# Optimization experiments

Measured on AMD Instinct MI355X. Metric: run time of the kernel, lower is better.

## Reference

```python
import jax, jax.numpy as jnp
import numpy as np

N_NODES = 100000
N_EDGES = 1600000
IN_DIM, HID_DIM, OUT_DIM = 128, 256, 128


def gcn_conv(x, src, dst, W, b, n):
    # PyG GCNConv: linear transform, add self-loops, symmetric normalization,
    # scatter-sum aggregation over destination nodes, then bias.
    h = x @ W  # [n, d_out]
    loops = jnp.arange(n, dtype=src.dtype)
    s = jnp.concatenate([src, loops])
    d = jnp.concatenate([dst, loops])
    deg = jax.ops.segment_sum(jnp.ones_like(d, dtype=h.dtype), d, num_segments=n)
    dinv = jnp.where(deg > 0, jax.lax.rsqrt(deg), 0.0)
    norm = dinv[s] * dinv[d]  # [E+n]
    msg = h[s] * norm[:, None]  # gather + scale
    out = jax.ops.segment_sum(msg, d, num_segments=n)  # scatter-reduce
    return out + b


def layer_norm(x, gamma, beta, eps=1e-5):
    mu = jnp.mean(x, axis=-1, keepdims=True)
    var = jnp.mean(jnp.square(x - mu), axis=-1, keepdims=True)
    return (x - mu) * jax.lax.rsqrt(var + eps) * gamma + beta


def setup_inputs() -> dict:
    key = jax.random.key(0)
    ks = jax.random.split(key, 8)
    x = jax.random.normal(ks[0], (N_NODES, IN_DIM), dtype=jnp.float32)
    edge_index = jax.random.randint(ks[1], (2, N_EDGES), 0, N_NODES, dtype=jnp.int64)
    W1 = jax.random.normal(ks[2], (IN_DIM, HID_DIM), dtype=jnp.float32) * (1.0 / np.sqrt(IN_DIM))
    b1 = jnp.zeros((HID_DIM,), dtype=jnp.float32)
    W2 = jax.random.normal(ks[3], (HID_DIM, OUT_DIM), dtype=jnp.float32) * (1.0 / np.sqrt(HID_DIM))
    b2 = jnp.zeros((OUT_DIM,), dtype=jnp.float32)
    gamma = jnp.ones((OUT_DIM,), dtype=jnp.float32)
    beta = jnp.zeros((OUT_DIM,), dtype=jnp.float32)
    return {"x": x, "edge_index": edge_index, "W1": W1, "b1": b1,
            "W2": W2, "b2": b2, "gamma": gamma, "beta": beta}


def reference(x, edge_index, W1, b1, W2, b2, gamma, beta):
    n = x.shape[0]
    src, dst = edge_index[0], edge_index[1]
    h = gcn_conv(x, src, dst, W1, b1, n)
    h = jax.nn.relu(h)
    # dropout(p=0.1) is identity in eval mode
    h = gcn_conv(h, src, dst, W2, b2, n)
    return layer_norm(h, gamma, beta)
```

## Files before the change

kernel.cpp:

```cpp
#include <hip/hip_runtime.h>
#include <hip/hip_fp16.h>
#include <stdint.h>

#define N_NODES 100000
#define N_EDGES 1600000
#define IN_DIM  128
#define HID_DIM 256
#define OUT_DIM 128
#define RS 264
#define NBUCK 391
#define EPB   4096
#define PADB  5120
#define PB    391
#define WB    256

typedef __attribute__((ext_vector_type(8))) _Float16 f16x8;
typedef __attribute__((ext_vector_type(4))) float f32x4;

__device__ __forceinline__ int clampi(int v) {
    v = v < 0 ? 0 : v;
    return v >= N_NODES ? N_NODES - 1 : v;
}
__device__ __forceinline__ float2 h2f2(uint32_t u) {
    union { uint32_t u; __half2 h; } c; c.u = u;
    return __half22float2(c.h);
}
__device__ __forceinline__ uint32_t packh(float a, float b) {
    union { __half2 h; uint32_t u; } c; c.h = __floats2half2_rn(a, b);
    return c.u;
}
__device__ __forceinline__ uint16_t f2h(float a) {
    union { __half h; uint16_t s; } c; c.h = __float2half_rn(a);
    return c.s;
}

__device__ __forceinline__ int src_at(const int* ei, int isI64, int e) {
    return clampi(isI64 ? ei[2 * (size_t)e] : ei[e]);
}
__device__ __forceinline__ int dst_at(const int* ei, int isI64, int e) {
    return clampi(isI64 ? ei[2 * (size_t)N_EDGES + 2 * (size_t)e]
                        : ei[(size_t)N_EDGES + e]);
}


__global__ __launch_bounds__(256) void partition_kernel(const int* __restrict__ ei,
                                                        int* __restrict__ cursor,
                                                        uint32_t* __restrict__ recs,
                                                        const float* __restrict__ W1,
                                                        uint16_t* __restrict__ W1t,
                                                        const float* __restrict__ W2,
                                                        uint16_t* __restrict__ W2t) {
    if (blockIdx.x >= PB) {
        int idx = (blockIdx.x - PB) * 256 + threadIdx.x;
        if (idx < IN_DIM * HID_DIM) {
            int k = idx / HID_DIM, n = idx - k * HID_DIM;
            W1t[n * IN_DIM + k] = f2h(W1[idx]);
        } else {
            int j = idx - IN_DIM * HID_DIM;
            int k = j / OUT_DIM, n = j - k * OUT_DIM;
            W2t[n * HID_DIM + k] = f2h(W2[j]);
        }
        return;
    }
    __shared__ int hist[NBUCK];
    __shared__ int gBase[NBUCK];
    __shared__ int s_flag;
    int tid = threadIdx.x;
    if (tid == 0) {
        int z = 1;
        #pragma unroll
        for (int i = 0; i < 16; ++i)
            if (ei[2 * i + 1] != 0) z = 0;
        s_flag = z;
    }
    for (int b = tid; b < NBUCK; b += 256) hist[b] = 0;
    __syncthreads();
    int isI64 = s_flag;
    int base = blockIdx.x * EPB;
    int srcs[16], dsts[16], slots[16];
    #pragma unroll
    for (int r = 0; r < 16; ++r) {
        int e = base + r * 256 + tid;
        slots[r] = -1;
        srcs[r] = 0; dsts[r] = 0;
        if (e < N_EDGES) {
            srcs[r] = src_at(ei, isI64, e);
            dsts[r] = dst_at(ei, isI64, e);
            slots[r] = atomicAdd(&hist[dsts[r] >> 8], 1);
        }
    }
    __syncthreads();
    for (int b = tid; b < NBUCK; b += 256)
        if (hist[b] > 0) gBase[b] = atomicAdd(&cursor[b], hist[b]);
    __syncthreads();
    #pragma unroll
    for (int r = 0; r < 16; ++r) {
        if (slots[r] >= 0) {
            int b = dsts[r] >> 8;
            int pos = gBase[b] + slots[r];
            if (pos < PADB)
                recs[(size_t)b * PADB + pos] =
                    ((uint32_t)srcs[r] << 8) | (uint32_t)(dsts[r] & 255);
        }
    }
}


__global__ __launch_bounds__(256) void build_kernel(const uint32_t* __restrict__ recs,
                                                    const int* __restrict__ cursor,
                                                    int* __restrict__ row_ptr,
                                                    float* __restrict__ dinv,
                                                    int* __restrict__ colv) {
    __shared__ int cnt[256];
    __shared__ int lofs[256];
    __shared__ int cur[256];
    __shared__ int wsum[8];
    int b = blockIdx.x, tid = threadIdx.x;
    int lane = tid & 63, wv = tid >> 6;
    int nb = cursor[b]; if (nb > PADB) nb = PADB;
    int pv = 0;
    for (int j = tid; j < b; j += 256) {
        int c = cursor[j];
        pv += (c > PADB) ? PADB : c;
    }
    #pragma unroll
    for (int o = 32; o > 0; o >>= 1) pv += __shfl_xor(pv, o, 64);
    cnt[tid] = 0; cur[tid] = 0;
    if (lane == 0) wsum[wv] = pv;
    __syncthreads();
    int cbase = wsum[0] + wsum[1] + wsum[2] + wsum[3];
    uint32_t rr[20];
    #pragma unroll
    for (int r = 0; r < 20; ++r) {
        int i = r * 256 + tid;
        rr[r] = 0xFFFFFFFFu;
        if (i < nb) {
            rr[r] = recs[(size_t)b * PADB + i];
            atomicAdd(&cnt[rr[r] & 255], 1);
        }
    }
    __syncthreads();
    int v = cnt[tid];
    int inc = v;
    #pragma unroll
    for (int o = 1; o < 64; o <<= 1) {
        int t = __shfl_up(inc, o, 64);
        if (lane >= o) inc += t;
    }
    if (lane == 63) wsum[4 + wv] = inc;
    __syncthreads();
    int woff = 0;
    #pragma unroll
    for (int w = 0; w < 4; ++w) if (w < wv) woff += wsum[4 + w];
    int excl = woff + inc - v;
    lofs[tid] = excl;
    int node = b * 256 + tid;
    if (node < N_NODES) {
        row_ptr[node] = cbase + excl;
        dinv[node] = rsqrtf((float)(v + 1));
    }
    if (b == NBUCK - 1 && tid == 0) row_ptr[N_NODES] = cbase + nb;
    __syncthreads();
    #pragma unroll
    for (int r = 0; r < 20; ++r) {
        if (rr[r] != 0xFFFFFFFFu) {
            int id = (int)(rr[r] & 255);
            int slot = atomicAdd(&cur[id], 1);
            colv[cbase + lofs[id] + slot] = (int)(rr[r] >> 8);
        }
    }
}


__global__ __launch_bounds__(256) void xscale_kernel(const float* __restrict__ x,
                                                     const float* __restrict__ dinv,
                                                     uint2* __restrict__ xs16) {
    int idx = blockIdx.x * 256 + threadIdx.x;
    if (idx < N_NODES * 32) {
        float d = dinv[idx >> 5];
        float4 v = ((const float4*)x)[idx];
        uint2 o;
        o.x = packh(d * v.x, d * v.y);
        o.y = packh(d * v.z, d * v.w);
        xs16[idx] = o;
    }
}


template<bool LN>
__global__ __launch_bounds__(256) void agg_kernel(const uint4* __restrict__ rows,
                                                  const int* __restrict__ row_ptr,
                                                  const int* __restrict__ colv,
                                                  const float* __restrict__ dinv,
                                                  const float* __restrict__ bias,
                                                  const float* __restrict__ gamma,
                                                  const float* __restrict__ beta,
                                                  float* __restrict__ out,
                                                  uint4* __restrict__ out16) {
    int node = blockIdx.x * 16 + (threadIdx.x >> 4);
    if (node >= N_NODES) return;
    int l = threadIdx.x & 15;
    const char* base = (const char*)rows + ((unsigned)l << 4);
    float di = dinv[node];
    float acc[8];
    {
        uint4 u = *(const uint4*)(base + ((unsigned)node << 8));
        float2 f0 = h2f2(u.x), f1 = h2f2(u.y), f2 = h2f2(u.z), f3 = h2f2(u.w);
        acc[0] = f0.x; acc[1] = f0.y; acc[2] = f1.x; acc[3] = f1.y;
        acc[4] = f2.x; acc[5] = f2.y; acc[6] = f3.x; acc[7] = f3.y;
    }
    int e = row_ptr[node], e1 = row_ptr[node + 1];
    int s0 = 0, s1 = 0, s2 = 0, s3 = 0;
    if (e     < e1) s0 = colv[e];
    if (e + 1 < e1) s1 = colv[e + 1];
    if (e + 2 < e1) s2 = colv[e + 2];
    if (e + 3 < e1) s3 = colv[e + 3];
    while (e + 4 <= e1) {
        uint4 v0 = *(const uint4*)(base + ((unsigned)s0 << 8));
        uint4 v1 = *(const uint4*)(base + ((unsigned)s1 << 8));
        uint4 v2 = *(const uint4*)(base + ((unsigned)s2 << 8));
        uint4 v3 = *(const uint4*)(base + ((unsigned)s3 << 8));
        int p0 = (e + 4 < e1) ? e + 4 : e;
        int p1 = (e + 5 < e1) ? e + 5 : e;
        int p2 = (e + 6 < e1) ? e + 6 : e;
        int p3 = (e + 7 < e1) ? e + 7 : e;
        int t0 = colv[p0], t1 = colv[p1], t2 = colv[p2], t3 = colv[p3];
        {
            float2 f0 = h2f2(v0.x), f1 = h2f2(v0.y), f2 = h2f2(v0.z), f3 = h2f2(v0.w);
            acc[0] += f0.x; acc[1] += f0.y; acc[2] += f1.x; acc[3] += f1.y;
            acc[4] += f2.x; acc[5] += f2.y; acc[6] += f3.x; acc[7] += f3.y;
        }
        {
            float2 f0 = h2f2(v1.x), f1 = h2f2(v1.y), f2 = h2f2(v1.z), f3 = h2f2(v1.w);
            acc[0] += f0.x; acc[1] += f0.y; acc[2] += f1.x; acc[3] += f1.y;
            acc[4] += f2.x; acc[5] += f2.y; acc[6] += f3.x; acc[7] += f3.y;
        }
        {
            float2 f0 = h2f2(v2.x), f1 = h2f2(v2.y), f2 = h2f2(v2.z), f3 = h2f2(v2.w);
            acc[0] += f0.x; acc[1] += f0.y; acc[2] += f1.x; acc[3] += f1.y;
            acc[4] += f2.x; acc[5] += f2.y; acc[6] += f3.x; acc[7] += f3.y;
        }
        {
            float2 f0 = h2f2(v3.x), f1 = h2f2(v3.y), f2 = h2f2(v3.z), f3 = h2f2(v3.w);
            acc[0] += f0.x; acc[1] += f0.y; acc[2] += f1.x; acc[3] += f1.y;
            acc[4] += f2.x; acc[5] += f2.y; acc[6] += f3.x; acc[7] += f3.y;
        }
        s0 = t0; s1 = t1; s2 = t2; s3 = t3; e += 4;
    }
    int r = e1 - e;
    if (r > 0) {
        uint4 v = *(const uint4*)(base + ((unsigned)s0 << 8));
        float2 f0 = h2f2(v.x), f1 = h2f2(v.y), f2 = h2f2(v.z), f3 = h2f2(v.w);
        acc[0] += f0.x; acc[1] += f0.y; acc[2] += f1.x; acc[3] += f1.y;
        acc[4] += f2.x; acc[5] += f2.y; acc[6] += f3.x; acc[7] += f3.y;
    }
    if (r > 1) {
        uint4 v = *(const uint4*)(base + ((unsigned)s1 << 8));
        float2 f0 = h2f2(v.x), f1 = h2f2(v.y), f2 = h2f2(v.z), f3 = h2f2(v.w);
        acc[0] += f0.x; acc[1] += f0.y; acc[2] += f1.x; acc[3] += f1.y;
        acc[4] += f2.x; acc[5] += f2.y; acc[6] += f3.x; acc[7] += f3.y;
    }
    if (r > 2) {
        uint4 v = *(const uint4*)(base + ((unsigned)s2 << 8));
        float2 f0 = h2f2(v.x), f1 = h2f2(v.y), f2 = h2f2(v.z), f3 = h2f2(v.w);
        acc[0] += f0.x; acc[1] += f0.y; acc[2] += f1.x; acc[3] += f1.y;
        acc[4] += f2.x; acc[5] += f2.y; acc[6] += f3.x; acc[7] += f3.y;
    }
    if (!LN) {
        uint4 o;
        o.x = packh(acc[0] * di, acc[1] * di);
        o.y = packh(acc[2] * di, acc[3] * di);
        o.z = packh(acc[4] * di, acc[5] * di);
        o.w = packh(acc[6] * di, acc[7] * di);
        out16[(size_t)node * 16 + l] = o;
    } else {
        const float4* b4 = (const float4*)(bias + l * 8);
        float4 bb0 = b4[0], bb1 = b4[1];
        float v[8];
        v[0] = acc[0] * di + bb0.x; v[1] = acc[1] * di + bb0.y;
        v[2] = acc[2] * di + bb0.z; v[3] = acc[3] * di + bb0.w;
        v[4] = acc[4] * di + bb1.x; v[5] = acc[5] * di + bb1.y;
        v[6] = acc[6] * di + bb1.z; v[7] = acc[7] * di + bb1.w;
        float s = 0.f;
        #pragma unroll
        for (int j = 0; j < 8; ++j) s += v[j];
        #pragma unroll
        for (int o = 8; o > 0; o >>= 1) s += __shfl_xor(s, o, 64);
        float mu = s * (1.0f / 128.0f);
        float q = 0.f;
        #pragma unroll
        for (int j = 0; j < 8; ++j) { v[j] -= mu; q += v[j] * v[j]; }
        #pragma unroll
        for (int o = 8; o > 0; o >>= 1) q += __shfl_xor(q, o, 64);
        float rstd = rsqrtf(q * (1.0f / 128.0f) + 1e-5f);
        const float4* g4 = (const float4*)(gamma + l * 8);
        const float4* t4 = (const float4*)(beta + l * 8);
        float4 g0 = g4[0], g1 = g4[1], t0 = t4[0], t1 = t4[1];
        float* orow = out + (size_t)node * 128 + l * 8;
        f32x4 o0, o1;
        o0.x = v[0] * rstd * g0.x + t0.x; o0.y = v[1] * rstd * g0.y + t0.y;
        o0.z = v[2] * rstd * g0.z + t0.z; o0.w = v[3] * rstd * g0.w + t0.w;
        o1.x = v[4] * rstd * g1.x + t1.x; o1.y = v[5] * rstd * g1.y + t1.y;
        o1.z = v[6] * rstd * g1.z + t1.z; o1.w = v[7] * rstd * g1.w + t1.w;
        __builtin_nontemporal_store(o0, (f32x4*)orow);
        __builtin_nontemporal_store(o1, (f32x4*)(orow + 4));
    }
}


__global__ __launch_bounds__(256) void fused_gemm_kernel(const uint16_t* __restrict__ A16,
                                                         const uint16_t* __restrict__ W1t,
                                                         const float* __restrict__ b1,
                                                         const uint16_t* __restrict__ W2t,
                                                         const float* __restrict__ dinv,
                                                         uint16_t* __restrict__ G16, int M) {
    __shared__ __align__(16) uint16_t Hs[64 * RS];
    int lane = threadIdx.x & 63;
    int wave = threadIdx.x >> 6;
    int r15 = lane & 15;
    int quad = lane >> 4;
    int kofs = quad * 8;
    int blk_row = blockIdx.x * 64;

    f16x8 a[4][4];
    #pragma unroll
    for (int mt = 0; mt < 4; ++mt) {
        bool valid = (blk_row + mt * 16) < M;
        int row = valid ? (blk_row + mt * 16 + r15) : 0;
        const uint16_t* arow = A16 + (size_t)row * IN_DIM + kofs;
        #pragma unroll
        for (int ks = 0; ks < 4; ++ks)
            a[mt][ks] = *(const f16x8*)(arow + ks * 32);
    }

    #pragma unroll
    for (int nt = 0; nt < 4; ++nt) {
        int ncol = (wave * 4 + nt) * 16 + r15;
        const uint16_t* bp = W1t + (size_t)ncol * IN_DIM + kofs;
        f32x4 acc[4];
        #pragma unroll
        for (int mt = 0; mt < 4; ++mt) acc[mt] = (f32x4){0.f, 0.f, 0.f, 0.f};
        #pragma unroll
        for (int ks = 0; ks < 4; ++ks) {
            f16x8 bv = *(const f16x8*)(bp + ks * 32);
            #pragma unroll
            for (int mt = 0; mt < 4; ++mt)
                acc[mt] = __builtin_amdgcn_mfma_f32_16x16x32_f16(a[mt][ks], bv, acc[mt], 0, 0, 0);
        }
        float bb = b1[ncol];
        #pragma unroll
        for (int mt = 0; mt < 4; ++mt) {
            #pragma unroll
            for (int r = 0; r < 4; ++r) {
                int lrow = mt * 16 + quad * 4 + r;
                Hs[lrow * RS + ncol] = f2h(fmaxf(acc[mt][r] + bb, 0.f));
            }
        }
    }
    __syncthreads();

    #pragma unroll
    for (int nt = 0; nt < 2; ++nt) {
        int ncol = (wave * 2 + nt) * 16 + r15;
        const uint16_t* bp = W2t + (size_t)ncol * HID_DIM + kofs;
        f16x8 b2[8];
        #pragma unroll
        for (int ks = 0; ks < 8; ++ks)
            b2[ks] = *(const f16x8*)(bp + ks * 32);
        f32x4 acc[4];
        #pragma unroll
        for (int mt = 0; mt < 4; ++mt) acc[mt] = (f32x4){0.f, 0.f, 0.f, 0.f};
        #pragma unroll
        for (int ks = 0; ks < 8; ++ks) {
            #pragma unroll
            for (int mt = 0; mt < 4; ++mt) {
                f16x8 av = *(const f16x8*)(Hs + (mt * 16 + r15) * RS + ks * 32 + kofs);
                acc[mt] = __builtin_amdgcn_mfma_f32_16x16x32_f16(av, b2[ks], acc[mt], 0, 0, 0);
            }
        }
        #pragma unroll
        for (int mt = 0; mt < 4; ++mt) {
            if ((blk_row + mt * 16) < M) {
                #pragma unroll
                for (int r = 0; r < 4; ++r) {
                    int row = blk_row + mt * 16 + quad * 4 + r;
                    G16[(size_t)row * OUT_DIM + ncol] = f2h(dinv[row] * acc[mt][r]);
                }
            }
        }
    }
}


extern "C" void kernel_launch(void* const* d_in, const int* in_sizes, int n_in,
                              void* d_out, int out_size, void* d_ws, size_t ws_size,
                              hipStream_t stream) {
    const float* x     = (const float*)d_in[0];
    const int*   ei    = (const int*)d_in[1];
    const float* W1    = (const float*)d_in[2];
    const float* b1    = (const float*)d_in[3];
    const float* W2    = (const float*)d_in[4];
    const float* b2    = (const float*)d_in[5];
    const float* gamma = (const float*)d_in[6];
    const float* beta  = (const float*)d_in[7];

    char* ws = (char*)d_ws;
    size_t off = 0;
    auto alloc = [&](size_t bytes) -> void* {
        void* p = ws + off;
        off += (bytes + 511) & ~(size_t)511;
        return p;
    };
    int*      cursor  = (int*)alloc((size_t)NBUCK * 4);
    int*      row_ptr = (int*)alloc((size_t)(N_NODES + 1) * 4);
    float*    dinv    = (float*)alloc((size_t)N_NODES * 4);
    uint16_t* W1t     = (uint16_t*)alloc((size_t)IN_DIM * HID_DIM * 2);
    uint16_t* W2t     = (uint16_t*)alloc((size_t)HID_DIM * OUT_DIM * 2);
    int*      colv    = (int*)alloc((size_t)N_EDGES * 4);
    void*     big     = alloc((size_t)N_NODES * IN_DIM * 2);
    uint32_t* recs    = (uint32_t*)big;
    uint16_t* g16     = (uint16_t*)big;
    if (ws_size < off) return;

    uint2*    xs16 = (uint2*)d_out;
    uint16_t* xa16 = (uint16_t*)d_out + (size_t)N_NODES * IN_DIM;

    const int AB = (N_NODES + 15) / 16;
    const int GB = (N_NODES + 63) / 64;
    const int XB = (N_NODES * 32 + 255) / 256;

    hipMemsetAsync(cursor, 0, (size_t)NBUCK * 4, stream);
    partition_kernel<<<PB + WB, 256, 0, stream>>>(ei, cursor, recs, W1, W1t, W2, W2t);
    build_kernel<<<NBUCK, 256, 0, stream>>>(recs, cursor, row_ptr, dinv, colv);
    xscale_kernel<<<XB, 256, 0, stream>>>(x, dinv, xs16);
    agg_kernel<false><<<AB, 256, 0, stream>>>((const uint4*)xs16, row_ptr, colv, dinv,
                                              nullptr, nullptr, nullptr,
                                              nullptr, (uint4*)xa16);
    fused_gemm_kernel<<<GB, 256, 0, stream>>>(xa16, W1t, b1, W2t, dinv, g16, N_NODES);
    agg_kernel<true><<<AB, 256, 0, stream>>>((const uint4*)g16, row_ptr, colv, dinv,
                                             b2, gamma, beta, (float*)d_out, nullptr);
}
```

Before: 316.7 us.

## Replace bucketed partition CSR build with global degree count, scan, atomic scatter

Swaps the two-pass bucket partition (per-block histogram into padded bucket records, then per-bucket local sort) for a classic CSR build: global atomic degree histogram, a two-kernel prefix scan, and an atomic-decrement scatter of source indices into colv. This removes the intermediate record buffer and the PADB overflow clamp, but adds two launches, reads the edge list twice, and relies on global atomics to random addresses. Column order within a row becomes nondeterministic, which may change floating-point summation order.

```diff
diff --git a/kernel.cpp b/kernel.cpp
--- a/kernel.cpp
+++ b/kernel.cpp
@@ -9,9 +9,7 @@
 #define OUT_DIM 128
 #define RS 264
 #define NBUCK 391
-#define EPB   4096
-#define PADB  5120
-#define PB    391
+#define DEGB  1563
 #define WB    256
 
 typedef __attribute__((ext_vector_type(8))) _Float16 f16x8;
@@ -43,15 +41,14 @@
 }
 
 
-__global__ __launch_bounds__(256) void partition_kernel(const int* __restrict__ ei,
-                                                        int* __restrict__ cursor,
-                                                        uint32_t* __restrict__ recs,
-                                                        const float* __restrict__ W1,
-                                                        uint16_t* __restrict__ W1t,
-                                                        const float* __restrict__ W2,
-                                                        uint16_t* __restrict__ W2t) {
-    if (blockIdx.x >= PB) {
-        int idx = (blockIdx.x - PB) * 256 + threadIdx.x;
+__global__ __launch_bounds__(256) void deg_kernel(const int* __restrict__ ei,
+                                                  int* __restrict__ deg,
+                                                  const float* __restrict__ W1,
+                                                  uint16_t* __restrict__ W1t,
+                                                  const float* __restrict__ W2,
+                                                  uint16_t* __restrict__ W2t) {
+    if (blockIdx.x >= DEGB) {
+        int idx = (blockIdx.x - DEGB) * 256 + threadIdx.x;
         if (idx < IN_DIM * HID_DIM) {
             int k = idx / HID_DIM, n = idx - k * HID_DIM;
             W1t[n * IN_DIM + k] = f2h(W1[idx]);
@@ -62,85 +59,56 @@
         }
         return;
     }
-    __shared__ int hist[NBUCK];
-    __shared__ int gBase[NBUCK];
     __shared__ int s_flag;
-    int tid = threadIdx.x;
-    if (tid == 0) {
+    if (threadIdx.x == 0) {
         int z = 1;
         #pragma unroll
         for (int i = 0; i < 16; ++i)
             if (ei[2 * i + 1] != 0) z = 0;
         s_flag = z;
     }
-    for (int b = tid; b < NBUCK; b += 256) hist[b] = 0;
     __syncthreads();
     int isI64 = s_flag;
-    int base = blockIdx.x * EPB;
-    int srcs[16], dsts[16], slots[16];
-    #pragma unroll
-    for (int r = 0; r < 16; ++r) {
-        int e = base + r * 256 + tid;
-        slots[r] = -1;
-        srcs[r] = 0; dsts[r] = 0;
-        if (e < N_EDGES) {
-            srcs[r] = src_at(ei, isI64, e);
-            dsts[r] = dst_at(ei, isI64, e);
-            slots[r] = atomicAdd(&hist[dsts[r] >> 8], 1);
-        }
-    }
-    __syncthreads();
-    for (int b = tid; b < NBUCK; b += 256)
-        if (hist[b] > 0) gBase[b] = atomicAdd(&cursor[b], hist[b]);
-    __syncthreads();
-    #pragma unroll
-    for (int r = 0; r < 16; ++r) {
-        if (slots[r] >= 0) {
-            int b = dsts[r] >> 8;
-            int pos = gBase[b] + slots[r];
-            if (pos < PADB)
-                recs[(size_t)b * PADB + pos] =
-                    ((uint32_t)srcs[r] << 8) | (uint32_t)(dsts[r] & 255);
-        }
-    }
-}
-
-
-__global__ __launch_bounds__(256) void build_kernel(const uint32_t* __restrict__ recs,
-                                                    const int* __restrict__ cursor,
+    int base = blockIdx.x * 1024 + threadIdx.x;
+    #pragma unroll
+    for (int r = 0; r < 4; ++r) {
+        int e = base + r * 256;
+        if (e < N_EDGES)
+            atomicAdd(&deg[dst_at(ei, isI64, e)], 1);
+    }
+}
+
+
+__global__ __launch_bounds__(256) void scanA_kernel(const int* __restrict__ deg,
+                                                    int* __restrict__ bsum) {
+    __shared__ int ws[4];
+    int b = blockIdx.x, tid = threadIdx.x, lane = tid & 63, wv = tid >> 6;
+    int node = b * 256 + tid;
+    int v = (node < N_NODES) ? deg[node] : 0;
+    #pragma unroll
+    for (int o = 32; o > 0; o >>= 1) v += __shfl_xor(v, o, 64);
+    if (lane == 0) ws[wv] = v;
+    __syncthreads();
+    if (tid == 0) bsum[b] = ws[0] + ws[1] + ws[2] + ws[3];
+}
+
+
+__global__ __launch_bounds__(256) void scanB_kernel(const int* __restrict__ deg,
+                                                    const int* __restrict__ bsum,
                                                     int* __restrict__ row_ptr,
-                                                    float* __restrict__ dinv,
-                                                    int* __restrict__ colv) {
-    __shared__ int cnt[256];
-    __shared__ int lofs[256];
-    __shared__ int cur[256];
+                                                    float* __restrict__ dinv) {
     __shared__ int wsum[8];
-    int b = blockIdx.x, tid = threadIdx.x;
-    int lane = tid & 63, wv = tid >> 6;
-    int nb = cursor[b]; if (nb > PADB) nb = PADB;
+    int b = blockIdx.x, tid = threadIdx.x, lane = tid & 63, wv = tid >> 6;
     int pv = 0;
-    for (int j = tid; j < b; j += 256) {
-        int c = cursor[j];
-        pv += (c > PADB) ? PADB : c;
-    }
+    for (int j = tid; j < b; j += 256) pv += bsum[j];
     #pragma unroll
     for (int o = 32; o > 0; o >>= 1) pv += __shfl_xor(pv, o, 64);
-    cnt[tid] = 0; cur[tid] = 0;
     if (lane == 0) wsum[wv] = pv;
     __syncthreads();
     int cbase = wsum[0] + wsum[1] + wsum[2] + wsum[3];
-    uint32_t rr[20];
-    #pragma unroll
-    for (int r = 0; r < 20; ++r) {
-        int i = r * 256 + tid;
-        rr[r] = 0xFFFFFFFFu;
-        if (i < nb) {
-            rr[r] = recs[(size_t)b * PADB + i];
-            atomicAdd(&cnt[rr[r] & 255], 1);
-        }
-    }
-    __syncthreads();
-    int v = cnt[tid];
+    __syncthreads();
+    int node = b * 256 + tid;
+    int v = (node < N_NODES) ? deg[node] : 0;
     int inc = v;
     #pragma unroll
     for (int o = 1; o < 64; o <<= 1) {
@@ -152,21 +120,38 @@
     int woff = 0;
     #pragma unroll
     for (int w = 0; w < 4; ++w) if (w < wv) woff += wsum[4 + w];
-    int excl = woff + inc - v;
-    lofs[tid] = excl;
-    int node = b * 256 + tid;
     if (node < N_NODES) {
-        row_ptr[node] = cbase + excl;
+        row_ptr[node] = cbase + woff + inc - v;
         dinv[node] = rsqrtf((float)(v + 1));
     }
-    if (b == NBUCK - 1 && tid == 0) row_ptr[N_NODES] = cbase + nb;
-    __syncthreads();
-    #pragma unroll
-    for (int r = 0; r < 20; ++r) {
-        if (rr[r] != 0xFFFFFFFFu) {
-            int id = (int)(rr[r] & 255);
-            int slot = atomicAdd(&cur[id], 1);
-            colv[cbase + lofs[id] + slot] = (int)(rr[r] >> 8);
+    if (b == NBUCK - 1 && tid == 0)
+        row_ptr[N_NODES] = cbase + wsum[4] + wsum[5] + wsum[6] + wsum[7];
+}
+
+
+__global__ __launch_bounds__(256) void scatter_kernel(const int* __restrict__ ei,
+                                                      int* __restrict__ deg,
+                                                      const int* __restrict__ row_ptr,
+                                                      int* __restrict__ colv) {
+    __shared__ int s_flag;
+    if (threadIdx.x == 0) {
+        int z = 1;
+        #pragma unroll
+        for (int i = 0; i < 16; ++i)
+            if (ei[2 * i + 1] != 0) z = 0;
+        s_flag = z;
+    }
+    __syncthreads();
+    int isI64 = s_flag;
+    int base = blockIdx.x * 1024 + threadIdx.x;
+    #pragma unroll
+    for (int r = 0; r < 4; ++r) {
+        int e = base + r * 256;
+        if (e < N_EDGES) {
+            int s = src_at(ei, isI64, e);
+            int d = dst_at(ei, isI64, e);
+            int slot = atomicSub(&deg[d], 1) - 1;
+            colv[row_ptr[d] + slot] = s;
         }
     }
 }
@@ -411,14 +396,14 @@
         off += (bytes + 511) & ~(size_t)511;
         return p;
     };
-    int*      cursor  = (int*)alloc((size_t)NBUCK * 4);
+    int*      deg     = (int*)alloc((size_t)N_NODES * 4);
+    int*      bsum    = (int*)alloc((size_t)NBUCK * 4);
     int*      row_ptr = (int*)alloc((size_t)(N_NODES + 1) * 4);
     float*    dinv    = (float*)alloc((size_t)N_NODES * 4);
     uint16_t* W1t     = (uint16_t*)alloc((size_t)IN_DIM * HID_DIM * 2);
     uint16_t* W2t     = (uint16_t*)alloc((size_t)HID_DIM * OUT_DIM * 2);
     int*      colv    = (int*)alloc((size_t)N_EDGES * 4);
     void*     big     = alloc((size_t)N_NODES * IN_DIM * 2);
-    uint32_t* recs    = (uint32_t*)big;
     uint16_t* g16     = (uint16_t*)big;
     if (ws_size < off) return;
 
@@ -429,10 +414,12 @@
     const int GB = (N_NODES + 63) / 64;
     const int XB = (N_NODES * 32 + 255) / 256;
 
-    hipMemsetAsync(cursor, 0, (size_t)NBUCK * 4, stream);
-    partition_kernel<<<PB + WB, 256, 0, stream>>>(ei, cursor, recs, W1, W1t, W2, W2t);
-    build_kernel<<<NBUCK, 256, 0, stream>>>(recs, cursor, row_ptr, dinv, colv);
+    hipMemsetAsync(deg, 0, (size_t)N_NODES * 4, stream);
+    deg_kernel<<<DEGB + WB, 256, 0, stream>>>(ei, deg, W1, W1t, W2, W2t);
+    scanA_kernel<<<NBUCK, 256, 0, stream>>>(deg, bsum);
+    scanB_kernel<<<NBUCK, 256, 0, stream>>>(deg, bsum, row_ptr, dinv);
     xscale_kernel<<<XB, 256, 0, stream>>>(x, dinv, xs16);
+    scatter_kernel<<<DEGB, 256, 0, stream>>>(ei, deg, row_ptr, colv);
     agg_kernel<false><<<AB, 256, 0, stream>>>((const uint4*)xs16, row_ptr, colv, dinv,
                                               nullptr, nullptr, nullptr,
                                               nullptr, (uint4*)xa16);
```

New measurement: 440.0 us. 1.39x slower.
